# Kernel optimization log

Measured on AMD Instinct MI355X. Metric: run time of the kernel, lower is better.

The kernel has to match this reference:

```python
import jax, jax.numpy as jnp
import numpy as np

B, C, H, W = 32, 64, 96, 96
RED = 8


def setup_inputs() -> dict:
    key = jax.random.key(0)
    k0, k1, k2 = jax.random.split(key, 3)
    x = jax.random.normal(k0, (B, C, H, W), dtype=jnp.float32)
    # 1x1 conv weights (squeezed to linear): conv1 C->C//RED, conv2 C//RED->C
    w1 = jax.random.normal(k1, (C // RED, C), dtype=jnp.float32) * (1.0 / np.sqrt(C))
    b1 = jnp.zeros((C // RED,), dtype=jnp.float32)
    w2 = jax.random.normal(k2, (C, C // RED), dtype=jnp.float32) * (1.0 / np.sqrt(C // RED))
    b2 = jnp.zeros((C,), dtype=jnp.float32)
    return {"x": x, "w1": w1, "b1": b1, "w2": w2, "b2": b2}


def reference(x, w1, b1, w2, b2):
    Bx, Cx, Hx, Wx = x.shape
    M = Hx * Wx
    # --- covariance pooling: x @ I_hat @ x^T == centered outer product / M ---
    xr = x.reshape(Bx, Cx, M)
    xc = xr - xr.mean(axis=-1, keepdims=True)
    cov = jnp.einsum('bcm,bdm->bcd', xc, xc) / M  # (B, C, C)
    # --- Newton-Schulz matrix sqrt, iteration = 5 ---
    I3 = 3.0 * jnp.eye(Cx, dtype=x.dtype)  # broadcast over batch
    normA = jnp.trace(cov, axis1=1, axis2=2)  # (1/3 * cov * 3I).sum == trace
    A = cov / normA[:, None, None]
    ZY = 0.5 * (I3 - A)
    Y = A @ ZY
    Z = ZY
    for _ in range(3):  # range(1, iteration-1) with iteration=5
        ZY = (0.5 * (I3 - Z)) @ Y
        Y = Y @ ZY
        Z = ZY @ Z
    ZY = 0.5 * (Y @ (I3 - Z @ Y))
    cov_sqrt = ZY * jnp.sqrt(normA)[:, None, None]  # (B, C, C)
    # --- channel gating ---
    s = cov_sqrt.mean(axis=1)  # mean over dim=1 -> (B, C)
    h = jax.nn.relu(s @ w1.T + b1)
    gate = jax.nn.sigmoid(h @ w2.T + b2)  # (B, C)
    return x * gate[:, :, None, None]
```

## Files before the change

### kernel.cpp

```cpp
#include <hip/hip_runtime.h>
#include <math.h>


#define BB 32
#define CC 64
#define MM 9216
#define NCHUNKS 16

typedef __attribute__((ext_vector_type(8))) short bf16x8;
typedef __attribute__((ext_vector_type(4))) float f32x4;

__device__ __forceinline__ short f2bf(float f) {
  unsigned u = __builtin_bit_cast(unsigned, f);
  return (short)(unsigned short)((u + 0x8000u) >> 16);
}
__device__ __forceinline__ float bf2f(short h) {
  unsigned u = ((unsigned)(unsigned short)h) << 16;
  return __builtin_bit_cast(float, u);
}

template <int NSTEP>
__device__ __forceinline__ void gram_body(const float* __restrict__ xb, int mwave,
                                          int quad, int col,
                                          f32x4 acc[4][4], float csum[4]) {
  const float* base[4];
#pragma unroll
  for (int rb = 0; rb < 4; rb++)
    base[rb] = xb + (size_t)(rb * 16 + col) * MM + mwave + quad * 8;

  float4 cur[4][2];
#pragma unroll
  for (int rb = 0; rb < 4; rb++) {
    cur[rb][0] = *(const float4*)(base[rb]);
    cur[rb][1] = *(const float4*)(base[rb] + 4);
  }
#pragma unroll
  for (int s = 0; s < NSTEP; s++) {
    float4 nxt[4][2];
    if (s + 1 < NSTEP) {
#pragma unroll
      for (int rb = 0; rb < 4; rb++) {
        const float* p = base[rb] + (s + 1) * 32;
        nxt[rb][0] = *(const float4*)(p);
        nxt[rb][1] = *(const float4*)(p + 4);
      }
    }
    bf16x8 frag[4];
#pragma unroll
    for (int rb = 0; rb < 4; rb++) {
      float v0 = cur[rb][0].x, v1 = cur[rb][0].y, v2 = cur[rb][0].z, v3 = cur[rb][0].w;
      float v4 = cur[rb][1].x, v5 = cur[rb][1].y, v6 = cur[rb][1].z, v7 = cur[rb][1].w;
      csum[rb] += ((v0 + v1) + (v2 + v3)) + ((v4 + v5) + (v6 + v7));
      bf16x8 f;
      f[0] = f2bf(v0); f[1] = f2bf(v1); f[2] = f2bf(v2); f[3] = f2bf(v3);
      f[4] = f2bf(v4); f[5] = f2bf(v5); f[6] = f2bf(v6); f[7] = f2bf(v7);
      frag[rb] = f;
    }
#pragma unroll
    for (int i = 0; i < 4; i++)
#pragma unroll
      for (int j = 0; j < 4; j++)
        acc[i][j] = __builtin_amdgcn_mfma_f32_16x16x32_bf16(frag[i], frag[j],
                                                            acc[i][j], 0, 0, 0);
    if (s + 1 < NSTEP) {
#pragma unroll
      for (int rb = 0; rb < 4; rb++) {
        cur[rb][0] = nxt[rb][0];
        cur[rb][1] = nxt[rb][1];
      }
    }
  }
}

template <bool PART>
__global__ __launch_bounds__(256, 2) void gram_k(const float* __restrict__ x,
                                                 float* __restrict__ pg,
                                                 float* __restrict__ ps) {
  int b = blockIdx.x / NCHUNKS;
  int chunk = blockIdx.x % NCHUNKS;
  int tid = threadIdx.x;
  int w = tid >> 6, lane = tid & 63;
  int quad = lane >> 4, col = lane & 15;
  const float* xb = x + (size_t)b * CC * MM;

  f32x4 acc[4][4];
#pragma unroll
  for (int i = 0; i < 4; i++)
#pragma unroll
    for (int j = 0; j < 4; j++) acc[i][j] = (f32x4){0.f, 0.f, 0.f, 0.f};
  float csum[4] = {0.f, 0.f, 0.f, 0.f};

  if (chunk < 8) {
    int mwave = chunk * 640 + w * (5 * 32);
    gram_body<5>(xb, mwave, quad, col, acc, csum);
  } else {
    int mwave = 5120 + (chunk - 8) * 512 + w * (4 * 32);
    gram_body<4>(xb, mwave, quad, col, acc, csum);
  }

  __shared__ float red[4][4096];
  __shared__ float cred[4][64];
#pragma unroll
  for (int i = 0; i < 4; i++)
#pragma unroll
    for (int j = 0; j < 4; j++)
#pragma unroll
      for (int r = 0; r < 4; r++)
        red[w][(i * 16 + quad * 4 + r) * 64 + j * 16 + col] = acc[i][j][r];
#pragma unroll
  for (int rb = 0; rb < 4; rb++) {
    float c0 = csum[rb];
    c0 += __shfl_xor(c0, 16);
    c0 += __shfl_xor(c0, 32);
    if (lane < 16) cred[w][rb * 16 + lane] = c0;
  }
  __syncthreads();

  if (PART) {
    float* covb = pg + (size_t)blockIdx.x * 4096;
#pragma unroll
    for (int e = 0; e < 16; e++) {
      int idx = tid + 256 * e;
      covb[idx] = (red[0][idx] + red[1][idx]) + (red[2][idx] + red[3][idx]);
    }
    if (tid < 64)
      ps[blockIdx.x * 64 + tid] =
          (cred[0][tid] + cred[1][tid]) + (cred[2][tid] + cred[3][tid]);
  } else {
    float* covb = pg + (size_t)b * 4096;
#pragma unroll
    for (int e = 0; e < 16; e++) {
      int idx = tid + 256 * e;
      float v = (red[0][idx] + red[1][idx]) + (red[2][idx] + red[3][idx]);
      atomicAdd(covb + idx, v);
    }
    if (tid < 64) {
      float v = (cred[0][tid] + cred[1][tid]) + (cred[2][tid] + cred[3][tid]);
      atomicAdd(ps + b * 64 + tid, v);
    }
  }
}

__device__ __forceinline__ void mm64(short* __restrict__ D, const short* __restrict__ A,
                                     const short* __restrict__ Bm, int tid) {
  int w = tid >> 6, lane = tid & 63, quad = lane >> 4, col = lane & 15;
  f32x4 acc[4];
#pragma unroll
  for (int j = 0; j < 4; j++) acc[j] = (f32x4){0.f, 0.f, 0.f, 0.f};
#pragma unroll
  for (int ks = 0; ks < 2; ks++) {
    int k0 = ks * 32 + quad * 8;
    bf16x8 fa = *(const bf16x8*)(A + (w * 16 + col) * 64 + k0);
#pragma unroll
    for (int j = 0; j < 4; j++) {
      bf16x8 fb = *(const bf16x8*)(Bm + (j * 16 + col) * 64 + k0);
      acc[j] = __builtin_amdgcn_mfma_f32_16x16x32_bf16(fa, fb, acc[j], 0, 0, 0);
    }
  }
#pragma unroll
  for (int j = 0; j < 4; j++)
#pragma unroll
    for (int r = 0; r < 4; r++)
      D[(w * 16 + quad * 4 + r) * 64 + j * 16 + col] = f2bf(acc[j][r]);
}

__device__ __forceinline__ void mmcolsum(const short* __restrict__ A,
                                         const short* __restrict__ Bm,
                                         float* scol, int tid) {
  int w = tid >> 6, lane = tid & 63, quad = lane >> 4, col = lane & 15;
  f32x4 acc[4];
#pragma unroll
  for (int j = 0; j < 4; j++) acc[j] = (f32x4){0.f, 0.f, 0.f, 0.f};
#pragma unroll
  for (int ks = 0; ks < 2; ks++) {
    int k0 = ks * 32 + quad * 8;
    bf16x8 fa = *(const bf16x8*)(A + (w * 16 + col) * 64 + k0);
#pragma unroll
    for (int j = 0; j < 4; j++) {
      bf16x8 fb = *(const bf16x8*)(Bm + (j * 16 + col) * 64 + k0);
      acc[j] = __builtin_amdgcn_mfma_f32_16x16x32_bf16(fa, fb, acc[j], 0, 0, 0);
    }
  }
#pragma unroll
  for (int j = 0; j < 4; j++) {
    float t = (acc[j][0] + acc[j][1]) + (acc[j][2] + acc[j][3]);
    atomicAdd(&scol[j * 16 + col], t);
  }
}

template <bool PART>
__global__ __launch_bounds__(256) void ns_k(const float* __restrict__ pg,
                                            const float* __restrict__ ps,
                                            const float* __restrict__ w1,
                                            const float* __restrict__ pb1,
                                            const float* __restrict__ w2,
                                            const float* __restrict__ pb2,
                                            float* __restrict__ gatews) {
  __shared__ __align__(16) short nb0[4096], nb1[4096], nb2[4096], nb3[4096], nb4[4096];
  __shared__ float gsum[4096];
  __shared__ float mu[64];
  __shared__ float scol[64];
  __shared__ float hbuf[8];
  __shared__ float normA_sh;
  int b = blockIdx.x;
  int tid = threadIdx.x;

  if (PART) {
    const float* pgb = pg + (size_t)b * NCHUNKS * 4096;
#pragma unroll
    for (int e = 0; e < 16; e++) {
      int idx = tid + 256 * e;
      float s = 0.f;
#pragma unroll
      for (int c = 0; c < NCHUNKS; c++) s += pgb[c * 4096 + idx];
      gsum[idx] = s;
    }
    if (tid < 64) {
      const float* psb = ps + (size_t)b * NCHUNKS * 64;
      float s = 0.f;
#pragma unroll
      for (int c = 0; c < NCHUNKS; c++) s += psb[c * 64 + tid];
      mu[tid] = s * (1.0f / MM);
    }
  } else {
    const float* gram = pg + (size_t)b * 4096;
#pragma unroll
    for (int e = 0; e < 16; e++) {
      int idx = tid + 256 * e;
      gsum[idx] = gram[idx];
    }
    if (tid < 64) mu[tid] = ps[b * 64 + tid] * (1.0f / MM);
  }
  __syncthreads();

  if (tid < 64) {
    float d = gsum[tid * 65] * (1.0f / MM) - mu[tid] * mu[tid];
#pragma unroll
    for (int off = 32; off >= 1; off >>= 1) d += __shfl_down(d, off);
    if (tid == 0) normA_sh = d;
  }
  __syncthreads();
  float normA = normA_sh;
  float rn = 1.0f / normA;
#pragma unroll
  for (int e = 0; e < 16; e++) {
    int idx = tid + 256 * e;
    int r = idx >> 6, c = idx & 63;
    float cv = gsum[idx] * (1.0f / MM) - mu[r] * mu[c];
    float a = cv * rn;
    nb0[idx] = f2bf(a);
    nb1[idx] = f2bf((r == c ? 1.5f : 0.0f) - 0.5f * a);
  }
  __syncthreads();
  mm64(nb2, nb0, nb1, tid);
  __syncthreads();
  short *pY = nb2, *pZ = nb1, *s0 = nb3, *s1 = nb4, *s2 = nb0;
  for (int it = 0; it < 3; ++it) {
#pragma unroll
    for (int e = 0; e < 16; e++) {
      int idx = tid + 256 * e;
      int r = idx >> 6, c = idx & 63;
      float z = bf2f(pZ[idx]);
      s0[idx] = f2bf((r == c ? 1.5f : 0.0f) - 0.5f * z);
    }
    __syncthreads();
    mm64(s1, s0, pY, tid);
    __syncthreads();
    mm64(s2, pY, s1, tid);
    mm64(s0, s1, pZ, tid);
    __syncthreads();
    short* oY = pY; short* oZ = pZ; short* oW = s1;
    pY = s2; pZ = s0; s0 = oY; s1 = oZ; s2 = oW;
  }
  mm64(s0, pZ, pY, tid);
  __syncthreads();
#pragma unroll
  for (int e = 0; e < 16; e++) {
    int idx = tid + 256 * e;
    int r = idx >> 6, c = idx & 63;
    float p = bf2f(s0[idx]);
    s0[idx] = f2bf((r == c ? 3.0f : 0.0f) - p);
  }
  if (tid < 64) scol[tid] = 0.0f;
  __syncthreads();
  mmcolsum(pY, s0, scol, tid);
  __syncthreads();
  if (tid < 8) {
    float sc = 0.5f * sqrtf(normA) * (1.0f / 64.0f);
    float acc2 = pb1[tid];
    for (int c = 0; c < 64; c++) acc2 += scol[c] * sc * w1[tid * 64 + c];
    hbuf[tid] = fmaxf(acc2, 0.0f);
  }
  __syncthreads();
  if (tid < 64) {
    float acc2 = pb2[tid];
#pragma unroll
    for (int j = 0; j < 8; j++) acc2 += hbuf[j] * w2[tid * 8 + j];
    gatews[b * 64 + tid] = 1.0f / (1.0f + __expf(-acc2));
  }
}

__global__ __launch_bounds__(256) void gate_mul(const float* __restrict__ x,
                                                const float* __restrict__ gatews,
                                                float* __restrict__ out) {
  int bc = blockIdx.x;
  float g = gatews[bc];
  const float4* xp = (const float4*)(x + (size_t)bc * MM);
  float4* op = (float4*)(out + (size_t)bc * MM);
  int t = threadIdx.x;
#pragma unroll
  for (int it = 0; it < 9; ++it) {
    float4 v = xp[t + it * 256];
    v.x *= g; v.y *= g; v.z *= g; v.w *= g;
    op[t + it * 256] = v;
  }
}

extern "C" void kernel_launch(void* const* d_in, const int* in_sizes, int n_in,
                              void* d_out, int out_size, void* d_ws, size_t ws_size,
                              hipStream_t stream) {
  const float* x = (const float*)d_in[0];
  const float* w1 = (const float*)d_in[1];
  const float* b1 = (const float*)d_in[2];
  const float* w2 = (const float*)d_in[3];
  const float* b2 = (const float*)d_in[4];
  float* out = (float*)d_out;
  float* ws = (float*)d_ws;

  const size_t NPG = (size_t)BB * NCHUNKS * 4096;
  const size_t NPS = (size_t)BB * NCHUNKS * 64;
  const size_t needP = (NPG + NPS + BB * CC) * sizeof(float);

  if (ws_size >= needP) {
    float* pg = ws;
    float* psum = ws + NPG;
    float* gatews = psum + NPS;
    gram_k<true><<<BB * NCHUNKS, 256, 0, stream>>>(x, pg, psum);
    ns_k<true><<<BB, 256, 0, stream>>>(pg, psum, w1, b1, w2, b2, gatews);
    gate_mul<<<BB * CC, 256, 0, stream>>>(x, gatews, out);
  } else {
    float* covws = ws;
    float* sumws = ws + BB * 4096;
    float* gatews = sumws + BB * 64;
    hipMemsetAsync(ws, 0, (size_t)(BB * 4096 + BB * 64) * sizeof(float), stream);
    gram_k<false><<<BB * NCHUNKS, 256, 0, stream>>>(x, covws, sumws);
    ns_k<false><<<BB, 256, 0, stream>>>(covws, sumws, w1, b1, w2, b2, gatews);
    gate_mul<<<BB * CC, 256, 0, stream>>>(x, gatews, out);
  }
}
```

Measured before the change: 168.7 us.

## Fuse Gram and Newton-Schulz kernels via last-block-done atomic counter

Merges the Gram partial-sum kernel and the Newton-Schulz/gating kernel into one launch. Each block writes its partials and increments a per-batch atomic counter, and the last-arriving block per batch runs the matrix-sqrt tail. The per-wave column sums are now written directly to global memory instead of being reduced in shared memory. This removes one kernel launch and its boundary, and lets the tail overlap with other batches' Gram work. In exchange it adds a memset, fences, and a 64KB shared buffer that may limit occupancy. The fallback path no longer uses atomics, but it needs the larger workspace layout that it does not check.

```diff
diff --git a/kernel.cpp b/kernel.cpp
--- a/kernel.cpp
+++ b/kernel.cpp
@@ -72,75 +72,6 @@
   }
 }
 
-template <bool PART>
-__global__ __launch_bounds__(256, 2) void gram_k(const float* __restrict__ x,
-                                                 float* __restrict__ pg,
-                                                 float* __restrict__ ps) {
-  int b = blockIdx.x / NCHUNKS;
-  int chunk = blockIdx.x % NCHUNKS;
-  int tid = threadIdx.x;
-  int w = tid >> 6, lane = tid & 63;
-  int quad = lane >> 4, col = lane & 15;
-  const float* xb = x + (size_t)b * CC * MM;
-
-  f32x4 acc[4][4];
-#pragma unroll
-  for (int i = 0; i < 4; i++)
-#pragma unroll
-    for (int j = 0; j < 4; j++) acc[i][j] = (f32x4){0.f, 0.f, 0.f, 0.f};
-  float csum[4] = {0.f, 0.f, 0.f, 0.f};
-
-  if (chunk < 8) {
-    int mwave = chunk * 640 + w * (5 * 32);
-    gram_body<5>(xb, mwave, quad, col, acc, csum);
-  } else {
-    int mwave = 5120 + (chunk - 8) * 512 + w * (4 * 32);
-    gram_body<4>(xb, mwave, quad, col, acc, csum);
-  }
-
-  __shared__ float red[4][4096];
-  __shared__ float cred[4][64];
-#pragma unroll
-  for (int i = 0; i < 4; i++)
-#pragma unroll
-    for (int j = 0; j < 4; j++)
-#pragma unroll
-      for (int r = 0; r < 4; r++)
-        red[w][(i * 16 + quad * 4 + r) * 64 + j * 16 + col] = acc[i][j][r];
-#pragma unroll
-  for (int rb = 0; rb < 4; rb++) {
-    float c0 = csum[rb];
-    c0 += __shfl_xor(c0, 16);
-    c0 += __shfl_xor(c0, 32);
-    if (lane < 16) cred[w][rb * 16 + lane] = c0;
-  }
-  __syncthreads();
-
-  if (PART) {
-    float* covb = pg + (size_t)blockIdx.x * 4096;
-#pragma unroll
-    for (int e = 0; e < 16; e++) {
-      int idx = tid + 256 * e;
-      covb[idx] = (red[0][idx] + red[1][idx]) + (red[2][idx] + red[3][idx]);
-    }
-    if (tid < 64)
-      ps[blockIdx.x * 64 + tid] =
-          (cred[0][tid] + cred[1][tid]) + (cred[2][tid] + cred[3][tid]);
-  } else {
-    float* covb = pg + (size_t)b * 4096;
-#pragma unroll
-    for (int e = 0; e < 16; e++) {
-      int idx = tid + 256 * e;
-      float v = (red[0][idx] + red[1][idx]) + (red[2][idx] + red[3][idx]);
-      atomicAdd(covb + idx, v);
-    }
-    if (tid < 64) {
-      float v = (cred[0][tid] + cred[1][tid]) + (cred[2][tid] + cred[3][tid]);
-      atomicAdd(ps + b * 64 + tid, v);
-    }
-  }
-}
-
 __device__ __forceinline__ void mm64(short* __restrict__ D, const short* __restrict__ A,
                                      const short* __restrict__ Bm, int tid) {
   int w = tid >> 6, lane = tid & 63, quad = lane >> 4, col = lane & 15;
@@ -188,24 +119,26 @@
   }
 }
 
-template <bool PART>
-__global__ __launch_bounds__(256) void ns_k(const float* __restrict__ pg,
-                                            const float* __restrict__ ps,
-                                            const float* __restrict__ w1,
-                                            const float* __restrict__ pb1,
-                                            const float* __restrict__ w2,
-                                            const float* __restrict__ pb2,
-                                            float* __restrict__ gatews) {
-  __shared__ __align__(16) short nb0[4096], nb1[4096], nb2[4096], nb3[4096], nb4[4096];
-  __shared__ float gsum[4096];
-  __shared__ float mu[64];
-  __shared__ float scol[64];
-  __shared__ float hbuf[8];
-  __shared__ float normA_sh;
-  int b = blockIdx.x;
-  int tid = threadIdx.x;
-
-  if (PART) {
+__device__ __forceinline__ void ns_tail(unsigned char* smem, int b, int tid,
+                                        const float* __restrict__ pg,
+                                        const float* __restrict__ ps,
+                                        const float* __restrict__ w1,
+                                        const float* __restrict__ pb1,
+                                        const float* __restrict__ w2,
+                                        const float* __restrict__ pb2,
+                                        float* __restrict__ gatews) {
+  short* nb0 = (short*)smem;
+  short* nb1 = nb0 + 4096;
+  short* nb2 = nb0 + 8192;
+  short* nb3 = nb0 + 12288;
+  short* nb4 = nb0 + 16384;
+  float* gsum = (float*)(smem + 40960);
+  float* mu = (float*)(smem + 57344);
+  float* scol = (float*)(smem + 57600);
+  float* hbuf = (float*)(smem + 57856);
+  float* pnorm = (float*)(smem + 57888);
+
+  {
     const float* pgb = pg + (size_t)b * NCHUNKS * 4096;
 #pragma unroll
     for (int e = 0; e < 16; e++) {
@@ -216,20 +149,14 @@
       gsum[idx] = s;
     }
     if (tid < 64) {
-      const float* psb = ps + (size_t)b * NCHUNKS * 64;
+      const float* psb = ps + (size_t)b * NCHUNKS * 256;
       float s = 0.f;
 #pragma unroll
-      for (int c = 0; c < NCHUNKS; c++) s += psb[c * 64 + tid];
+      for (int c = 0; c < NCHUNKS; c++)
+#pragma unroll
+        for (int sub = 0; sub < 4; sub++) s += psb[c * 256 + sub * 64 + tid];
       mu[tid] = s * (1.0f / MM);
     }
-  } else {
-    const float* gram = pg + (size_t)b * 4096;
-#pragma unroll
-    for (int e = 0; e < 16; e++) {
-      int idx = tid + 256 * e;
-      gsum[idx] = gram[idx];
-    }
-    if (tid < 64) mu[tid] = ps[b * 64 + tid] * (1.0f / MM);
   }
   __syncthreads();
 
@@ -237,10 +164,10 @@
     float d = gsum[tid * 65] * (1.0f / MM) - mu[tid] * mu[tid];
 #pragma unroll
     for (int off = 32; off >= 1; off >>= 1) d += __shfl_down(d, off);
-    if (tid == 0) normA_sh = d;
-  }
-  __syncthreads();
-  float normA = normA_sh;
+    if (tid == 0) *pnorm = d;
+  }
+  __syncthreads();
+  float normA = *pnorm;
   float rn = 1.0f / normA;
 #pragma unroll
   for (int e = 0; e < 16; e++) {
@@ -300,6 +227,74 @@
   }
 }
 
+__global__ __launch_bounds__(256, 2) void gramns_k(
+    const float* __restrict__ x, float* __restrict__ pg, float* __restrict__ ps,
+    int* __restrict__ ctr, const float* __restrict__ w1,
+    const float* __restrict__ pb1, const float* __restrict__ w2,
+    const float* __restrict__ pb2, float* __restrict__ gatews) {
+  __shared__ __align__(16) unsigned char smem[65536];
+  float(*red)[4096] = reinterpret_cast<float(*)[4096]>(smem);
+
+  int b = blockIdx.x / NCHUNKS;
+  int chunk = blockIdx.x % NCHUNKS;
+  int tid = threadIdx.x;
+  int w = tid >> 6, lane = tid & 63;
+  int quad = lane >> 4, col = lane & 15;
+  const float* xb = x + (size_t)b * CC * MM;
+
+  f32x4 acc[4][4];
+#pragma unroll
+  for (int i = 0; i < 4; i++)
+#pragma unroll
+    for (int j = 0; j < 4; j++) acc[i][j] = (f32x4){0.f, 0.f, 0.f, 0.f};
+  float csum[4] = {0.f, 0.f, 0.f, 0.f};
+
+  if (chunk < 8) {
+    int mwave = chunk * 640 + w * (5 * 32);
+    gram_body<5>(xb, mwave, quad, col, acc, csum);
+  } else {
+    int mwave = 5120 + (chunk - 8) * 512 + w * (4 * 32);
+    gram_body<4>(xb, mwave, quad, col, acc, csum);
+  }
+
+#pragma unroll
+  for (int rb = 0; rb < 4; rb++) {
+    float c0 = csum[rb];
+    c0 += __shfl_xor(c0, 16);
+    c0 += __shfl_xor(c0, 32);
+    if (lane < 16)
+      ps[(size_t)blockIdx.x * 256 + w * 64 + rb * 16 + lane] = c0;
+  }
+
+#pragma unroll
+  for (int i = 0; i < 4; i++)
+#pragma unroll
+    for (int j = 0; j < 4; j++)
+#pragma unroll
+      for (int r = 0; r < 4; r++)
+        red[w][(i * 16 + quad * 4 + r) * 64 + j * 16 + col] = acc[i][j][r];
+  __syncthreads();
+  float* covb = pg + (size_t)blockIdx.x * 4096;
+#pragma unroll
+  for (int e = 0; e < 16; e++) {
+    int idx = tid + 256 * e;
+    covb[idx] = (red[0][idx] + red[1][idx]) + (red[2][idx] + red[3][idx]);
+  }
+
+  __threadfence();
+  __syncthreads();
+  volatile int* pold = (int*)smem;
+  if (tid == 0)
+    *pold = __hip_atomic_fetch_add(ctr + b, 1, __ATOMIC_ACQ_REL,
+                                   __HIP_MEMORY_SCOPE_AGENT);
+  __syncthreads();
+  if (*pold != NCHUNKS - 1) return;
+  __threadfence();
+  __syncthreads();
+
+  ns_tail(smem, b, tid, pg, ps, w1, pb1, w2, pb2, gatews);
+}
+
 __global__ __launch_bounds__(256) void gate_mul(const float* __restrict__ x,
                                                 const float* __restrict__ gatews,
                                                 float* __restrict__ out) {
@@ -314,6 +309,65 @@
     v.x *= g; v.y *= g; v.z *= g; v.w *= g;
     op[t + it * 256] = v;
   }
+}
+
+__global__ __launch_bounds__(256, 2) void gram_k_leg(const float* __restrict__ x,
+                                                     float* __restrict__ pg,
+                                                     float* __restrict__ ps) {
+  int b = blockIdx.x / NCHUNKS;
+  int chunk = blockIdx.x % NCHUNKS;
+  int tid = threadIdx.x;
+  int w = tid >> 6, lane = tid & 63;
+  int quad = lane >> 4, col = lane & 15;
+  const float* xb = x + (size_t)b * CC * MM;
+
+  f32x4 acc[4][4];
+#pragma unroll
+  for (int i = 0; i < 4; i++)
+#pragma unroll
+    for (int j = 0; j < 4; j++) acc[i][j] = (f32x4){0.f, 0.f, 0.f, 0.f};
+  float csum[4] = {0.f, 0.f, 0.f, 0.f};
+  if (chunk < 8) {
+    int mwave = chunk * 640 + w * (5 * 32);
+    gram_body<5>(xb, mwave, quad, col, acc, csum);
+  } else {
+    int mwave = 5120 + (chunk - 8) * 512 + w * (4 * 32);
+    gram_body<4>(xb, mwave, quad, col, acc, csum);
+  }
+#pragma unroll
+  for (int rb = 0; rb < 4; rb++) {
+    float c0 = csum[rb];
+    c0 += __shfl_xor(c0, 16);
+    c0 += __shfl_xor(c0, 32);
+    if (lane < 16)
+      ps[(size_t)blockIdx.x * 256 + w * 64 + rb * 16 + lane] = c0;
+  }
+  __shared__ float red[4][4096];
+#pragma unroll
+  for (int i = 0; i < 4; i++)
+#pragma unroll
+    for (int j = 0; j < 4; j++)
+#pragma unroll
+      for (int r = 0; r < 4; r++)
+        red[w][(i * 16 + quad * 4 + r) * 64 + j * 16 + col] = acc[i][j][r];
+  __syncthreads();
+  float* covb = pg + (size_t)blockIdx.x * 4096;
+#pragma unroll
+  for (int e = 0; e < 16; e++) {
+    int idx = tid + 256 * e;
+    covb[idx] = (red[0][idx] + red[1][idx]) + (red[2][idx] + red[3][idx]);
+  }
+}
+
+__global__ __launch_bounds__(256) void ns_k_leg(const float* __restrict__ pg,
+                                                const float* __restrict__ ps,
+                                                const float* __restrict__ w1,
+                                                const float* __restrict__ pb1,
+                                                const float* __restrict__ w2,
+                                                const float* __restrict__ pb2,
+                                                float* __restrict__ gatews) {
+  __shared__ __align__(16) unsigned char smem[60416];
+  ns_tail(smem, blockIdx.x, threadIdx.x, pg, ps, w1, pb1, w2, pb2, gatews);
 }
 
 extern "C" void kernel_launch(void* const* d_in, const int* in_sizes, int n_in,
@@ -328,23 +382,21 @@
   float* ws = (float*)d_ws;
 
   const size_t NPG = (size_t)BB * NCHUNKS * 4096;
-  const size_t NPS = (size_t)BB * NCHUNKS * 64;
-  const size_t needP = (NPG + NPS + BB * CC) * sizeof(float);
+  const size_t NPS = (size_t)BB * NCHUNKS * 256;
+  float* pg = ws;
+  float* psum = ws + NPG;
+  int* ctr = (int*)(psum + NPS);
+  float* gatews = (float*)(ctr + BB);
+  const size_t needP = (NPG + NPS + BB + BB * CC) * sizeof(float);
 
   if (ws_size >= needP) {
-    float* pg = ws;
-    float* psum = ws + NPG;
-    float* gatews = psum + NPS;
-    gram_k<true><<<BB * NCHUNKS, 256, 0, stream>>>(x, pg, psum);
-    ns_k<true><<<BB, 256, 0, stream>>>(pg, psum, w1, b1, w2, b2, gatews);
+    hipMemsetAsync(ctr, 0, BB * sizeof(int), stream);
+    gramns_k<<<BB * NCHUNKS, 256, 0, stream>>>(x, pg, psum, ctr, w1, b1, w2,
+                                               b2, gatews);
     gate_mul<<<BB * CC, 256, 0, stream>>>(x, gatews, out);
   } else {
-    float* covws = ws;
-    float* sumws = ws + BB * 4096;
-    float* gatews = sumws + BB * 64;
-    hipMemsetAsync(ws, 0, (size_t)(BB * 4096 + BB * 64) * sizeof(float), stream);
-    gram_k<false><<<BB * NCHUNKS, 256, 0, stream>>>(x, covws, sumws);
-    ns_k<false><<<BB, 256, 0, stream>>>(covws, sumws, w1, b1, w2, b2, gatews);
+    gram_k_leg<<<BB * NCHUNKS, 256, 0, stream>>>(x, pg, psum);
+    ns_k_leg<<<BB, 256, 0, stream>>>(pg, psum, w1, b1, w2, b2, gatews);
     gate_mul<<<BB * CC, 256, 0, stream>>>(x, gatews, out);
   }
 }
```

Result: slower. 263.1 us (+56.0%).
